# Kernel tuning notes

Hardware: AMD Instinct MI355X
Metric: run time of the kernel (lower is better)

The kernel has to match this reference:

```python
import jax, jax.numpy as jnp
import numpy as np

N_HEAD = 16
D_MODEL = 1024
D_K = 64
D_V = 64
EPS = 1e-6

def setup_inputs() -> dict:
    key = jax.random.key(0)
    ks = jax.random.split(key, 9)
    B, S = 4, 2048
    sc = 0.02
    return {
        "q": jax.random.normal(ks[0], (B, S, D_MODEL), jnp.float32),
        "k": jax.random.normal(ks[1], (B, S, D_MODEL), jnp.float32),
        "v": jax.random.normal(ks[2], (B, S, D_MODEL), jnp.float32),
        # torch Linear weights: [out_features, in_features], y = x @ W.T
        "w_qs": jax.random.normal(ks[3], (N_HEAD * D_K, D_MODEL), jnp.float32) * sc,
        "w_ks": jax.random.normal(ks[4], (N_HEAD * D_K, D_MODEL), jnp.float32) * sc,
        "w_vs": jax.random.normal(ks[5], (N_HEAD * D_V, D_MODEL), jnp.float32) * sc,
        "w_fc": jax.random.normal(ks[6], (D_MODEL, N_HEAD * D_V), jnp.float32) * sc,
        "gamma": jnp.ones((D_MODEL,), jnp.float32),
        "beta": jnp.zeros((D_MODEL,), jnp.float32),
    }

def reference(q, k, v, w_qs, w_ks, w_vs, w_fc, gamma, beta):
    B, S, _ = q.shape
    residual = q
    # Faithful to original: .view(b, n_head, s, d_k) with NO transpose,
    # i.e. reinterpret (s, h*dk) as (h, s, dk).
    qh = (q @ w_qs.T).reshape(B, N_HEAD, S, D_K)
    kh = (k @ w_ks.T).reshape(B, N_HEAD, S, D_K)
    vh = (v @ w_vs.T).reshape(B, N_HEAD, S, D_V)
    # scaled dot-product attention (dropout inactive at eval)
    scores = jnp.einsum('bhqd,bhkd->bhqk', qh, kh) / jnp.sqrt(
        jnp.asarray(D_K, qh.dtype))
    attn = jax.nn.softmax(scores, axis=-1)
    ctx = jnp.einsum('bhqk,bhkd->bhqd', attn, vh)        # [B,H,S,Dv]
    ctx = ctx.transpose(0, 2, 1, 3).reshape(B, S, N_HEAD * D_V)
    output = ctx @ w_fc.T
    x = output + residual
    mu = jnp.mean(x, axis=-1, keepdims=True)
    var = jnp.var(x, axis=-1, keepdims=True)
    out = (x - mu) * jax.lax.rsqrt(var + EPS) * gamma + beta
    return out, attn
```

## Files before the change

### kernel.cpp

```cpp
#include <hip/hip_runtime.h>

#define S 2048
#define DM 1024
#define NH 16
#define DK 64
#define BATCH 4

typedef float f4 __attribute__((ext_vector_type(4)));
typedef __bf16 bf16x8 __attribute__((ext_vector_type(8)));

#define MFMA(a, b, c) __builtin_amdgcn_mfma_f32_16x16x32_bf16(a, b, c, 0, 0, 0)

__device__ __forceinline__ unsigned short f2bf(float f) {
  union { float f; unsigned int u; } x; x.f = f;
  return (unsigned short)((x.u + 0x7FFFu + ((x.u >> 16) & 1u)) >> 16);
}

__device__ __forceinline__ unsigned int pack2(float a, float b) {
  return (unsigned int)f2bf(a) | ((unsigned int)f2bf(b) << 16);
}

__device__ __forceinline__ void stage8(const float* __restrict__ src,
                                       unsigned short* dst) {
  float4 a = ((const float4*)src)[0];
  float4 b = ((const float4*)src)[1];
  uint4 p;
  p.x = pack2(a.x, a.y); p.y = pack2(a.z, a.w);
  p.z = pack2(b.x, b.y); p.w = pack2(b.z, b.w);
  *(uint4*)dst = p;
}

__device__ __forceinline__ void stage16bf(const unsigned short* __restrict__ src,
                                          unsigned short* dst) {
  uint4 a = ((const uint4*)src)[0];
  uint4 b = ((const uint4*)src)[1];
  ((uint4*)dst)[0] = a;
  ((uint4*)dst)[1] = b;
}

template <bool OUT_BF16, bool RES>
__global__ __launch_bounds__(256)
void gemm_xwt(const float* __restrict__ X, const float* __restrict__ W,
              const float* __restrict__ res, void* __restrict__ Yv,
              int M, int N, int K) {
  const int LDA = 40;
  __shared__ alignas(16) unsigned short As[128 * LDA];
  __shared__ alignas(16) unsigned short Bs[128 * LDA];

  const int tid = threadIdx.x;
  const int wid = tid >> 6, lane = tid & 63;
  const int g = lane >> 4, c = lane & 15;
  const int m0 = blockIdx.y * 128, n0 = blockIdx.x * 128;
  const int wm = (wid >> 1) * 64, wn = (wid & 1) * 64;

  f4 acc[4][4];
#pragma unroll
  for (int i = 0; i < 4; i++)
#pragma unroll
    for (int j = 0; j < 4; j++) acc[i][j] = (f4){0.f, 0.f, 0.f, 0.f};

  const int srow = tid >> 2;
  const int sk = (tid & 3) * 8;

  for (int k0 = 0; k0 < K; k0 += 32) {
#pragma unroll
    for (int rr = 0; rr < 128; rr += 64) {
      stage8(X + (size_t)(m0 + srow + rr) * K + k0 + sk,
             &As[(srow + rr) * LDA + sk]);
      stage8(W + (size_t)(n0 + srow + rr) * K + k0 + sk,
             &Bs[(srow + rr) * LDA + sk]);
    }
    __syncthreads();
    bf16x8 av[4], bv[4];
#pragma unroll
    for (int i = 0; i < 4; i++)
      av[i] = *(const bf16x8*)&As[(wm + i * 16 + c) * LDA + g * 8];
#pragma unroll
    for (int j = 0; j < 4; j++)
      bv[j] = *(const bf16x8*)&Bs[(wn + j * 16 + c) * LDA + g * 8];
#pragma unroll
    for (int i = 0; i < 4; i++)
#pragma unroll
      for (int j = 0; j < 4; j++)
        acc[i][j] = MFMA(av[i], bv[j], acc[i][j]);
    __syncthreads();
  }

#pragma unroll
  for (int i = 0; i < 4; i++) {
#pragma unroll
    for (int j = 0; j < 4; j++) {
      const int row = m0 + wm + i * 16 + g * 4;
      const int col = n0 + wn + j * 16 + c;
#pragma unroll
      for (int r = 0; r < 4; r++) {
        size_t off = (size_t)(row + r) * N + col;
        float vv = acc[i][j][r];
        if constexpr (RES) vv += res[off];
        if constexpr (OUT_BF16)
          ((unsigned short*)Yv)[off] = f2bf(vv);
        else
          ((float*)Yv)[off] = vv;
      }
    }
  }
}

__global__ __launch_bounds__(256)
void attn_kernel(const unsigned short* __restrict__ Qp,
                 const unsigned short* __restrict__ Kp,
                 const unsigned short* __restrict__ Vp,
                 float* __restrict__ attnOut, float* __restrict__ ctxOut) {
  const int LDA = 72;
  __shared__ alignas(16) unsigned short Qs[64 * LDA];
  __shared__ alignas(16) unsigned short Ks[64 * LDA];
  __shared__ alignas(16) unsigned short Vt[64 * LDA];
  __shared__ alignas(16) unsigned short Ps[4][16 * LDA];

  const int tid = threadIdx.x;
  const int wid = tid >> 6, lane = tid & 63;
  const int g = lane >> 4, c = lane & 15;

  const int bid = blockIdx.x;
  const int qb = bid & 31;
  const int h = (bid >> 5) & 15;
  const int b = bid >> 9;

  const size_t headOff = ((size_t)b * NH + h) * S * DK;
  const unsigned short* Qh = Qp + headOff;
  const unsigned short* Kh = Kp + headOff;
  const unsigned short* Vh = Vp + headOff;
  float* attnB = attnOut + (((size_t)b * NH + h) * S + (size_t)qb * 64) * S;

  const int srow = tid >> 2;
  const int sd = (tid & 3) * 16;

  stage16bf(Qh + (size_t)(qb * 64 + srow) * DK + sd, &Qs[srow * LDA + sd]);
  __syncthreads();

  const bf16x8 qa0 = *(const bf16x8*)&Qs[(wid * 16 + c) * LDA + g * 8];
  const bf16x8 qa1 = *(const bf16x8*)&Qs[(wid * 16 + c) * LDA + 32 + g * 8];

  float mrow[4], lrow[4];
#pragma unroll
  for (int r = 0; r < 4; r++) { mrow[r] = -1e30f; lrow[r] = 0.f; }

  const float scale = 0.125f;

  for (int kt = 0; kt < 32; kt++) {
    __syncthreads();
    stage16bf(Kh + (size_t)(kt * 64 + srow) * DK + sd, &Ks[srow * LDA + sd]);
    __syncthreads();

    f4 sf[4];
#pragma unroll
    for (int f = 0; f < 4; f++) {
      bf16x8 b0 = *(const bf16x8*)&Ks[(f * 16 + c) * LDA + g * 8];
      bf16x8 b1 = *(const bf16x8*)&Ks[(f * 16 + c) * LDA + 32 + g * 8];
      f4 s = (f4){0.f, 0.f, 0.f, 0.f};
      s = MFMA(qa0, b0, s);
      s = MFMA(qa1, b1, s);
      sf[f] = s * scale;
    }
    float tm[4], ps[4];
#pragma unroll
    for (int r = 0; r < 4; r++)
      tm[r] = fmaxf(fmaxf(sf[0][r], sf[1][r]), fmaxf(sf[2][r], sf[3][r]));
#pragma unroll
    for (int mask = 1; mask < 16; mask <<= 1)
#pragma unroll
      for (int r = 0; r < 4; r++)
        tm[r] = fmaxf(tm[r], __shfl_xor(tm[r], mask));
#pragma unroll
    for (int r = 0; r < 4; r++) {
      float nm = fmaxf(mrow[r], tm[r]);
      ps[r] = __expf(sf[0][r] - nm) + __expf(sf[1][r] - nm) +
              __expf(sf[2][r] - nm) + __expf(sf[3][r] - nm);
      lrow[r] = lrow[r] * __expf(mrow[r] - nm);
      mrow[r] = nm;
    }
#pragma unroll
    for (int mask = 1; mask < 16; mask <<= 1)
#pragma unroll
      for (int r = 0; r < 4; r++) ps[r] += __shfl_xor(ps[r], mask);
#pragma unroll
    for (int r = 0; r < 4; r++) lrow[r] += ps[r];
  }

  float rl[4];
#pragma unroll
  for (int r = 0; r < 4; r++) rl[r] = 1.f / lrow[r];

  f4 ctxv[4];
#pragma unroll
  for (int f = 0; f < 4; f++) ctxv[f] = (f4){0.f, 0.f, 0.f, 0.f};

  const int vk = tid & 63;
  const int vd = (tid >> 6) * 16;

  for (int kt = 0; kt < 32; kt++) {
    __syncthreads();
    stage16bf(Kh + (size_t)(kt * 64 + srow) * DK + sd, &Ks[srow * LDA + sd]);
    {
      const unsigned short* vp = Vh + (size_t)(kt * 64 + vk) * DK + vd;
      uint4 a = ((const uint4*)vp)[0];
      uint4 bq = ((const uint4*)vp)[1];
      unsigned short vals[16];
      vals[0] = a.x & 0xFFFF;  vals[1] = a.x >> 16;
      vals[2] = a.y & 0xFFFF;  vals[3] = a.y >> 16;
      vals[4] = a.z & 0xFFFF;  vals[5] = a.z >> 16;
      vals[6] = a.w & 0xFFFF;  vals[7] = a.w >> 16;
      vals[8] = bq.x & 0xFFFF; vals[9] = bq.x >> 16;
      vals[10] = bq.y & 0xFFFF; vals[11] = bq.y >> 16;
      vals[12] = bq.z & 0xFFFF; vals[13] = bq.z >> 16;
      vals[14] = bq.w & 0xFFFF; vals[15] = bq.w >> 16;
#pragma unroll
      for (int i = 0; i < 16; i++) Vt[(vd + i) * LDA + vk] = vals[i];
    }
    __syncthreads();

    f4 pf[4];
#pragma unroll
    for (int f = 0; f < 4; f++) {
      bf16x8 b0 = *(const bf16x8*)&Ks[(f * 16 + c) * LDA + g * 8];
      bf16x8 b1 = *(const bf16x8*)&Ks[(f * 16 + c) * LDA + 32 + g * 8];
      f4 s = (f4){0.f, 0.f, 0.f, 0.f};
      s = MFMA(qa0, b0, s);
      s = MFMA(qa1, b1, s);
#pragma unroll
      for (int r = 0; r < 4; r++)
        pf[f][r] = __expf(s[r] * scale - mrow[r]) * rl[r];
    }
    float* ap = attnB + (size_t)(wid * 16 + g * 4) * S + kt * 64;
#pragma unroll
    for (int f = 0; f < 4; f++)
#pragma unroll
      for (int r = 0; r < 4; r++)
        ap[(size_t)r * S + f * 16 + c] = pf[f][r];
#pragma unroll
    for (int f = 0; f < 4; f++)
#pragma unroll
      for (int r = 0; r < 4; r++)
        Ps[wid][(g * 4 + r) * LDA + f * 16 + c] = f2bf(pf[f][r]);
    __syncthreads();

    bf16x8 pa0 = *(const bf16x8*)&Ps[wid][c * LDA + g * 8];
    bf16x8 pa1 = *(const bf16x8*)&Ps[wid][c * LDA + 32 + g * 8];
#pragma unroll
    for (int f = 0; f < 4; f++) {
      bf16x8 v0 = *(const bf16x8*)&Vt[(f * 16 + c) * LDA + g * 8];
      bf16x8 v1 = *(const bf16x8*)&Vt[(f * 16 + c) * LDA + 32 + g * 8];
      ctxv[f] = MFMA(pa0, v0, ctxv[f]);
      ctxv[f] = MFMA(pa1, v1, ctxv[f]);
    }
  }

  float* cp = ctxOut +
              ((size_t)b * S + (size_t)qb * 64 + wid * 16 + g * 4) * DM + h * 64;
#pragma unroll
  for (int f = 0; f < 4; f++)
#pragma unroll
    for (int r = 0; r < 4; r++)
      cp[(size_t)r * DM + f * 16 + c] = ctxv[f][r];
}

__global__ __launch_bounds__(256)
void ln_kernel(float* __restrict__ X, const float* __restrict__ gamma,
               const float* __restrict__ beta) {
  __shared__ float ws[4], ws2[4];
  const int row = blockIdx.x;
  const int tid = threadIdx.x;
  const int wid = tid >> 6, lane = tid & 63;
  float* xp = X + (size_t)row * DM + tid * 4;
  float4 v = *(const float4*)xp;
  float s = v.x + v.y + v.z + v.w;
  float s2 = v.x * v.x + v.y * v.y + v.z * v.z + v.w * v.w;
#pragma unroll
  for (int m = 1; m < 64; m <<= 1) {
    s += __shfl_xor(s, m);
    s2 += __shfl_xor(s2, m);
  }
  if (lane == 0) { ws[wid] = s; ws2[wid] = s2; }
  __syncthreads();
  s = ws[0] + ws[1] + ws[2] + ws[3];
  s2 = ws2[0] + ws2[1] + ws2[2] + ws2[3];
  const float mean = s * (1.f / 1024.f);
  const float var = s2 * (1.f / 1024.f) - mean * mean;
  const float rstd = rsqrtf(var + 1e-6f);
  float4 gg = *(const float4*)(gamma + tid * 4);
  float4 bb = *(const float4*)(beta + tid * 4);
  float4 o;
  o.x = (v.x - mean) * rstd * gg.x + bb.x;
  o.y = (v.y - mean) * rstd * gg.y + bb.y;
  o.z = (v.z - mean) * rstd * gg.z + bb.z;
  o.w = (v.w - mean) * rstd * gg.w + bb.w;
  *(float4*)xp = o;
}

extern "C" void kernel_launch(void* const* d_in, const int* in_sizes, int n_in,
                              void* d_out, int out_size, void* d_ws,
                              size_t ws_size, hipStream_t stream) {
  const float* q = (const float*)d_in[0];
  const float* k = (const float*)d_in[1];
  const float* v = (const float*)d_in[2];
  const float* w_qs = (const float*)d_in[3];
  const float* w_ks = (const float*)d_in[4];
  const float* w_vs = (const float*)d_in[5];
  const float* w_fc = (const float*)d_in[6];
  const float* gamma = (const float*)d_in[7];
  const float* beta = (const float*)d_in[8];

  const size_t projN = (size_t)BATCH * S * DM;
  float* out = (float*)d_out;
  float* attnO = out + projN;

  unsigned short* Qp = (unsigned short*)d_ws;
  unsigned short* Kp = Qp + projN;
  unsigned short* Vp = Kp + projN;
  float* Ctx = (float*)(Vp + projN);

  const int M = BATCH * S;
  dim3 gg(DM / 128, M / 128);

  gemm_xwt<true, false><<<gg, 256, 0, stream>>>(q, w_qs, nullptr, Qp, M, DM, DM);
  gemm_xwt<true, false><<<gg, 256, 0, stream>>>(k, w_ks, nullptr, Kp, M, DM, DM);
  gemm_xwt<true, false><<<gg, 256, 0, stream>>>(v, w_vs, nullptr, Vp, M, DM, DM);

  attn_kernel<<<BATCH * NH * (S / 64), 256, 0, stream>>>(Qp, Kp, Vp, attnO, Ctx);

  gemm_xwt<false, true><<<gg, 256, 0, stream>>>(Ctx, w_fc, q, out, M, DM, DM);

  ln_kernel<<<M, 256, 0, stream>>>(out, gamma, beta);
}
```

Measured before the change: 1.625 ms.

## Pre-convert inputs to bf16, use direct global-to-LDS GEMM loads, double-buffer V in attention

Adds a conversion kernel that turns the weights and activations into bf16 before each projection. The GEMM now loads tiles with global_load_lds at K-step 64, drops the padded LDS stride, and remaps workgroups in an XCD-aware swizzle. The attention kernel reads K straight from global memory instead of staging it in LDS, double-buffers the transposed V tile with a packed transpose write and fewer barriers, swizzles block order, and writes the context as bf16 so the output projection reads half the bytes. The extra conversion passes add memory traffic and launches. The unpadded LDS layout in the GEMM may cause bank conflicts.

```diff
diff --git a/kernel.cpp b/kernel.cpp
--- a/kernel.cpp
+++ b/kernel.cpp
@@ -20,69 +20,82 @@
   return (unsigned int)f2bf(a) | ((unsigned int)f2bf(b) << 16);
 }
 
-__device__ __forceinline__ void stage8(const float* __restrict__ src,
-                                       unsigned short* dst) {
-  float4 a = ((const float4*)src)[0];
-  float4 b = ((const float4*)src)[1];
-  uint4 p;
-  p.x = pack2(a.x, a.y); p.y = pack2(a.z, a.w);
-  p.z = pack2(b.x, b.y); p.w = pack2(b.z, b.w);
-  *(uint4*)dst = p;
-}
-
-__device__ __forceinline__ void stage16bf(const unsigned short* __restrict__ src,
-                                          unsigned short* dst) {
-  uint4 a = ((const uint4*)src)[0];
-  uint4 b = ((const uint4*)src)[1];
-  ((uint4*)dst)[0] = a;
-  ((uint4*)dst)[1] = b;
+__global__ __launch_bounds__(256)
+void cvt_kernel(const float* __restrict__ in, unsigned short* __restrict__ out,
+                int n8) {
+  int i = blockIdx.x * 256 + threadIdx.x;
+  const int stride = gridDim.x * 256;
+  for (; i < n8; i += stride) {
+    const float4* p = (const float4*)in + 2 * (size_t)i;
+    float4 a = p[0], b = p[1];
+    uint4 o;
+    o.x = pack2(a.x, a.y); o.y = pack2(a.z, a.w);
+    o.z = pack2(b.x, b.y); o.w = pack2(b.z, b.w);
+    ((uint4*)out)[i] = o;
+  }
+}
+
+__device__ __forceinline__ void gl_lds16(const unsigned short* g,
+                                         unsigned short* l) {
+  __builtin_amdgcn_global_load_lds(
+      (const __attribute__((address_space(1))) unsigned int*)g,
+      (__attribute__((address_space(3))) unsigned int*)l, 16, 0, 0);
 }
 
 template <bool OUT_BF16, bool RES>
 __global__ __launch_bounds__(256)
-void gemm_xwt(const float* __restrict__ X, const float* __restrict__ W,
-              const float* __restrict__ res, void* __restrict__ Yv,
-              int M, int N, int K) {
-  const int LDA = 40;
-  __shared__ alignas(16) unsigned short As[128 * LDA];
-  __shared__ alignas(16) unsigned short Bs[128 * LDA];
+void gemm_bf(const unsigned short* __restrict__ X,
+             const unsigned short* __restrict__ W,
+             const float* __restrict__ res, void* __restrict__ Yv,
+             int M_, int N_, int K_) {
+  __shared__ alignas(16) unsigned short As[128 * 64];
+  __shared__ alignas(16) unsigned short Bs[128 * 64];
 
   const int tid = threadIdx.x;
   const int wid = tid >> 6, lane = tid & 63;
   const int g = lane >> 4, c = lane & 15;
-  const int m0 = blockIdx.y * 128, n0 = blockIdx.x * 128;
+
+  const int nwg = gridDim.x;
+  const int wg = blockIdx.x;
+  const int lb = (wg & 7) * (nwg >> 3) + (wg >> 3);
+  const int nbx = N_ >> 7;
+  const int m0 = (lb / nbx) << 7, n0 = (lb % nbx) << 7;
   const int wm = (wid >> 1) * 64, wn = (wid & 1) * 64;
 
+  const int lrow = lane >> 3;
+  const int lk = (lane & 7) * 8;
+  const unsigned short* xa = X + (size_t)(m0 + wid * 32 + lrow) * K_ + lk;
+  const unsigned short* wb = W + (size_t)(n0 + wid * 32 + lrow) * K_ + lk;
+  unsigned short* asb = &As[(wid * 32) * 64];
+  unsigned short* bsb = &Bs[(wid * 32) * 64];
+
   f4 acc[4][4];
 #pragma unroll
   for (int i = 0; i < 4; i++)
 #pragma unroll
     for (int j = 0; j < 4; j++) acc[i][j] = (f4){0.f, 0.f, 0.f, 0.f};
 
-  const int srow = tid >> 2;
-  const int sk = (tid & 3) * 8;
-
-  for (int k0 = 0; k0 < K; k0 += 32) {
-#pragma unroll
-    for (int rr = 0; rr < 128; rr += 64) {
-      stage8(X + (size_t)(m0 + srow + rr) * K + k0 + sk,
-             &As[(srow + rr) * LDA + sk]);
-      stage8(W + (size_t)(n0 + srow + rr) * K + k0 + sk,
-             &Bs[(srow + rr) * LDA + sk]);
+  for (int k0 = 0; k0 < K_; k0 += 64) {
+#pragma unroll
+    for (int j = 0; j < 4; j++) {
+      gl_lds16(xa + (size_t)j * 8 * K_ + k0, asb + j * 8 * 64);
+      gl_lds16(wb + (size_t)j * 8 * K_ + k0, bsb + j * 8 * 64);
     }
     __syncthreads();
-    bf16x8 av[4], bv[4];
-#pragma unroll
-    for (int i = 0; i < 4; i++)
-      av[i] = *(const bf16x8*)&As[(wm + i * 16 + c) * LDA + g * 8];
-#pragma unroll
-    for (int j = 0; j < 4; j++)
-      bv[j] = *(const bf16x8*)&Bs[(wn + j * 16 + c) * LDA + g * 8];
-#pragma unroll
-    for (int i = 0; i < 4; i++)
+#pragma unroll
+    for (int ks = 0; ks < 2; ks++) {
+      bf16x8 av[4], bv[4];
+#pragma unroll
+      for (int i = 0; i < 4; i++)
+        av[i] = *(const bf16x8*)&As[(wm + i * 16 + c) * 64 + ks * 32 + g * 8];
 #pragma unroll
       for (int j = 0; j < 4; j++)
-        acc[i][j] = MFMA(av[i], bv[j], acc[i][j]);
+        bv[j] = *(const bf16x8*)&Bs[(wn + j * 16 + c) * 64 + ks * 32 + g * 8];
+#pragma unroll
+      for (int i = 0; i < 4; i++)
+#pragma unroll
+        for (int j = 0; j < 4; j++) acc[i][j] = MFMA(av[i], bv[j], acc[i][j]);
+    }
     __syncthreads();
   }
 
@@ -94,7 +107,7 @@
       const int col = n0 + wn + j * 16 + c;
 #pragma unroll
       for (int r = 0; r < 4; r++) {
-        size_t off = (size_t)(row + r) * N + col;
+        size_t off = (size_t)(row + r) * N_ + col;
         float vv = acc[i][j][r];
         if constexpr (RES) vv += res[off];
         if constexpr (OUT_BF16)
@@ -106,22 +119,37 @@
   }
 }
 
+__device__ __forceinline__ void vwrite(unsigned short* VtBuf, int kpair,
+                                       int dblk, uint4 r0, uint4 r1) {
+  const int LDA = 72;
+  unsigned int lo[4] = {r0.x, r0.y, r0.z, r0.w};
+  unsigned int hi[4] = {r1.x, r1.y, r1.z, r1.w};
+#pragma unroll
+  for (int p = 0; p < 4; p++) {
+    unsigned int w0 = (lo[p] & 0xFFFFu) | (hi[p] << 16);
+    unsigned int w1 = (lo[p] >> 16) | (hi[p] & 0xFFFF0000u);
+    *(unsigned int*)&VtBuf[(dblk + 2 * p) * LDA + kpair] = w0;
+    *(unsigned int*)&VtBuf[(dblk + 2 * p + 1) * LDA + kpair] = w1;
+  }
+}
+
 __global__ __launch_bounds__(256)
 void attn_kernel(const unsigned short* __restrict__ Qp,
                  const unsigned short* __restrict__ Kp,
                  const unsigned short* __restrict__ Vp,
-                 float* __restrict__ attnOut, float* __restrict__ ctxOut) {
+                 float* __restrict__ attnOut,
+                 unsigned short* __restrict__ ctxOut) {
   const int LDA = 72;
   __shared__ alignas(16) unsigned short Qs[64 * LDA];
-  __shared__ alignas(16) unsigned short Ks[64 * LDA];
-  __shared__ alignas(16) unsigned short Vt[64 * LDA];
+  __shared__ alignas(16) unsigned short Vt[2][64 * LDA];
   __shared__ alignas(16) unsigned short Ps[4][16 * LDA];
 
   const int tid = threadIdx.x;
   const int wid = tid >> 6, lane = tid & 63;
   const int g = lane >> 4, c = lane & 15;
 
-  const int bid = blockIdx.x;
+  const int wg = blockIdx.x;
+  const int bid = (wg & 7) * (int)(gridDim.x >> 3) + (wg >> 3);
   const int qb = bid & 31;
   const int h = (bid >> 5) & 15;
   const int b = bid >> 9;
@@ -132,31 +160,31 @@
   const unsigned short* Vh = Vp + headOff;
   float* attnB = attnOut + (((size_t)b * NH + h) * S + (size_t)qb * 64) * S;
 
-  const int srow = tid >> 2;
-  const int sd = (tid & 3) * 16;
-
-  stage16bf(Qh + (size_t)(qb * 64 + srow) * DK + sd, &Qs[srow * LDA + sd]);
+  const int srow = tid >> 2, sd = (tid & 3) * 16;
+  {
+    const unsigned short* src = Qh + (size_t)(qb * 64 + srow) * DK + sd;
+    uint4 a = ((const uint4*)src)[0];
+    uint4 bq = ((const uint4*)src)[1];
+    ((uint4*)&Qs[srow * LDA + sd])[0] = a;
+    ((uint4*)&Qs[srow * LDA + sd])[1] = bq;
+  }
   __syncthreads();
-
   const bf16x8 qa0 = *(const bf16x8*)&Qs[(wid * 16 + c) * LDA + g * 8];
   const bf16x8 qa1 = *(const bf16x8*)&Qs[(wid * 16 + c) * LDA + 32 + g * 8];
 
   float mrow[4], lrow[4];
 #pragma unroll
   for (int r = 0; r < 4; r++) { mrow[r] = -1e30f; lrow[r] = 0.f; }
-
   const float scale = 0.125f;
 
   for (int kt = 0; kt < 32; kt++) {
-    __syncthreads();
-    stage16bf(Kh + (size_t)(kt * 64 + srow) * DK + sd, &Ks[srow * LDA + sd]);
-    __syncthreads();
-
+    const unsigned short* kb = Kh + (size_t)kt * 64 * DK;
     f4 sf[4];
 #pragma unroll
     for (int f = 0; f < 4; f++) {
-      bf16x8 b0 = *(const bf16x8*)&Ks[(f * 16 + c) * LDA + g * 8];
-      bf16x8 b1 = *(const bf16x8*)&Ks[(f * 16 + c) * LDA + 32 + g * 8];
+      const unsigned short* kr = kb + (size_t)(f * 16 + c) * DK + g * 8;
+      bf16x8 b0 = *(const bf16x8*)kr;
+      bf16x8 b1 = *(const bf16x8*)(kr + 32);
       f4 s = (f4){0.f, 0.f, 0.f, 0.f};
       s = MFMA(qa0, b0, s);
       s = MFMA(qa1, b1, s);
@@ -195,35 +223,34 @@
 #pragma unroll
   for (int f = 0; f < 4; f++) ctxv[f] = (f4){0.f, 0.f, 0.f, 0.f};
 
-  const int vk = tid & 63;
-  const int vd = (tid >> 6) * 16;
+  const int kpair = (tid & 31) * 2;
+  const int dblk = (tid >> 5) * 8;
+
+  {
+    const unsigned short* p0 = Vh + (size_t)kpair * DK + dblk;
+    uint4 r0 = *(const uint4*)p0;
+    uint4 r1 = *(const uint4*)(p0 + DK);
+    vwrite(Vt[0], kpair, dblk, r0, r1);
+  }
+  __syncthreads();
 
   for (int kt = 0; kt < 32; kt++) {
-    __syncthreads();
-    stage16bf(Kh + (size_t)(kt * 64 + srow) * DK + sd, &Ks[srow * LDA + sd]);
-    {
-      const unsigned short* vp = Vh + (size_t)(kt * 64 + vk) * DK + vd;
-      uint4 a = ((const uint4*)vp)[0];
-      uint4 bq = ((const uint4*)vp)[1];
-      unsigned short vals[16];
-      vals[0] = a.x & 0xFFFF;  vals[1] = a.x >> 16;
-      vals[2] = a.y & 0xFFFF;  vals[3] = a.y >> 16;
-      vals[4] = a.z & 0xFFFF;  vals[5] = a.z >> 16;
-      vals[6] = a.w & 0xFFFF;  vals[7] = a.w >> 16;
-      vals[8] = bq.x & 0xFFFF; vals[9] = bq.x >> 16;
-      vals[10] = bq.y & 0xFFFF; vals[11] = bq.y >> 16;
-      vals[12] = bq.z & 0xFFFF; vals[13] = bq.z >> 16;
-      vals[14] = bq.w & 0xFFFF; vals[15] = bq.w >> 16;
-#pragma unroll
-      for (int i = 0; i < 16; i++) Vt[(vd + i) * LDA + vk] = vals[i];
-    }
-    __syncthreads();
-
+    const int cur = kt & 1;
+    const bool pre = (kt < 31);
+    uint4 r0, r1;
+    if (pre) {
+      const unsigned short* p0 =
+          Vh + (size_t)((kt + 1) * 64 + kpair) * DK + dblk;
+      r0 = *(const uint4*)p0;
+      r1 = *(const uint4*)(p0 + DK);
+    }
+    const unsigned short* kb = Kh + (size_t)kt * 64 * DK;
     f4 pf[4];
 #pragma unroll
     for (int f = 0; f < 4; f++) {
-      bf16x8 b0 = *(const bf16x8*)&Ks[(f * 16 + c) * LDA + g * 8];
-      bf16x8 b1 = *(const bf16x8*)&Ks[(f * 16 + c) * LDA + 32 + g * 8];
+      const unsigned short* kr = kb + (size_t)(f * 16 + c) * DK + g * 8;
+      bf16x8 b0 = *(const bf16x8*)kr;
+      bf16x8 b1 = *(const bf16x8*)(kr + 32);
       f4 s = (f4){0.f, 0.f, 0.f, 0.f};
       s = MFMA(qa0, b0, s);
       s = MFMA(qa1, b1, s);
@@ -242,26 +269,27 @@
 #pragma unroll
       for (int r = 0; r < 4; r++)
         Ps[wid][(g * 4 + r) * LDA + f * 16 + c] = f2bf(pf[f][r]);
-    __syncthreads();
-
     bf16x8 pa0 = *(const bf16x8*)&Ps[wid][c * LDA + g * 8];
     bf16x8 pa1 = *(const bf16x8*)&Ps[wid][c * LDA + 32 + g * 8];
+    if (pre) vwrite(Vt[cur ^ 1], kpair, dblk, r0, r1);
 #pragma unroll
     for (int f = 0; f < 4; f++) {
-      bf16x8 v0 = *(const bf16x8*)&Vt[(f * 16 + c) * LDA + g * 8];
-      bf16x8 v1 = *(const bf16x8*)&Vt[(f * 16 + c) * LDA + 32 + g * 8];
+      bf16x8 v0 = *(const bf16x8*)&Vt[cur][(f * 16 + c) * LDA + g * 8];
+      bf16x8 v1 = *(const bf16x8*)&Vt[cur][(f * 16 + c) * LDA + 32 + g * 8];
       ctxv[f] = MFMA(pa0, v0, ctxv[f]);
       ctxv[f] = MFMA(pa1, v1, ctxv[f]);
     }
-  }
-
-  float* cp = ctxOut +
-              ((size_t)b * S + (size_t)qb * 64 + wid * 16 + g * 4) * DM + h * 64;
+    __syncthreads();
+  }
+
+  unsigned short* cp =
+      ctxOut + ((size_t)b * S + (size_t)qb * 64 + wid * 16 + g * 4) * DM +
+      h * 64;
 #pragma unroll
   for (int f = 0; f < 4; f++)
 #pragma unroll
     for (int r = 0; r < 4; r++)
-      cp[(size_t)r * DM + f * 16 + c] = ctxv[f][r];
+      cp[(size_t)r * DM + f * 16 + c] = f2bf(ctxv[f][r]);
 }
 
 __global__ __launch_bounds__(256)
@@ -311,24 +339,36 @@
   const float* beta = (const float*)d_in[8];
 
   const size_t projN = (size_t)BATCH * S * DM;
+  const size_t wN = (size_t)DM * DM;
   float* out = (float*)d_out;
   float* attnO = out + projN;
 
   unsigned short* Qp = (unsigned short*)d_ws;
   unsigned short* Kp = Qp + projN;
   unsigned short* Vp = Kp + projN;
-  float* Ctx = (float*)(Vp + projN);
+  unsigned short* XB = Vp + projN;
+  unsigned short* WQ = XB + projN;
+  unsigned short* WK = WQ + wN;
+  unsigned short* WV = WK + wN;
+  unsigned short* WF = WV + wN;
 
   const int M = BATCH * S;
-  dim3 gg(DM / 128, M / 128);
-
-  gemm_xwt<true, false><<<gg, 256, 0, stream>>>(q, w_qs, nullptr, Qp, M, DM, DM);
-  gemm_xwt<true, false><<<gg, 256, 0, stream>>>(k, w_ks, nullptr, Kp, M, DM, DM);
-  gemm_xwt<true, false><<<gg, 256, 0, stream>>>(v, w_vs, nullptr, Vp, M, DM, DM);
-
-  attn_kernel<<<BATCH * NH * (S / 64), 256, 0, stream>>>(Qp, Kp, Vp, attnO, Ctx);
-
-  gemm_xwt<false, true><<<gg, 256, 0, stream>>>(Ctx, w_fc, q, out, M, DM, DM);
-
+  const int GG = (M / 128) * (DM / 128);
+
+  cvt_kernel<<<512, 256, 0, stream>>>(w_qs, WQ, (int)(wN / 8));
+  cvt_kernel<<<512, 256, 0, stream>>>(w_ks, WK, (int)(wN / 8));
+  cvt_kernel<<<512, 256, 0, stream>>>(w_vs, WV, (int)(wN / 8));
+  cvt_kernel<<<512, 256, 0, stream>>>(w_fc, WF, (int)(wN / 8));
+
+  cvt_kernel<<<2048, 256, 0, stream>>>(q, XB, (int)(projN / 8));
+  gemm_bf<true, false><<<GG, 256, 0, stream>>>(XB, WQ, nullptr, Qp, M, DM, DM);
+  cvt_kernel<<<2048, 256, 0, stream>>>(k, XB, (int)(projN / 8));
+  gemm_bf<true, false><<<GG, 256, 0, stream>>>(XB, WK, nullptr, Kp, M, DM, DM);
+  cvt_kernel<<<2048, 256, 0, stream>>>(v, XB, (int)(projN / 8));
+  gemm_bf<true, false><<<GG, 256, 0, stream>>>(XB, WV, nullptr, Vp, M, DM, DM);
+
+  attn_kernel<<<BATCH * NH * (S / 64), 256, 0, stream>>>(Qp, Kp, Vp, attnO, XB);
+
+  gemm_bf<false, true><<<GG, 256, 0, stream>>>(XB, WF, q, out, M, DM, DM);
   ln_kernel<<<M, 256, 0, stream>>>(out, gamma, beta);
 }
```

Result: slower. 1.769 ms (+8.8%).
